# Kernel tuning notes

Measured on AMD Instinct MI355X. Metric: run time of the kernel, lower is better.

The kernel has to match this reference:

```python
import jax, jax.numpy as jnp
import numpy as np

N_EMBD = 1024
NUM_HEADS = 16
HEAD_SIZE = 64


def setup_inputs() -> dict:
    key = jax.random.key(0)
    ks = jax.random.split(key, 6)
    B, T, C, hs = 2, 2048, N_EMBD, HEAD_SIZE
    s = 0.02
    return {
        "x": jax.random.normal(ks[0], (B, T, C), dtype=jnp.float32),
        "Wk": jax.random.normal(ks[1], (hs, C), dtype=jnp.float32) * s,  # torch Linear weight [out,in]
        "Wv": jax.random.normal(ks[2], (hs, C), dtype=jnp.float32) * s,
        "Wq": jax.random.normal(ks[3], (C, C), dtype=jnp.float32) * s,
        "Wp": jax.random.normal(ks[4], (C, C), dtype=jnp.float32) * s,
        "bp": jax.random.normal(ks[5], (C,), dtype=jnp.float32) * s,
    }


def reference(x, Wk, Wv, Wq, Wp, bp):
    B, T, C = x.shape
    H, hs = NUM_HEADS, HEAD_SIZE
    k = x @ Wk.T                      # [B,T,hs]
    v = x @ Wv.T                      # [B,T,hs]
    q = x @ Wq.T                      # [B,T,C]
    # Faithful to torch: raw view of [B,T,C] -> [B,H,T,hs] (row-major reshape, not transpose)
    q = q.reshape(B, H, T, hs)
    k = k.reshape(B, 1, T, hs)
    v = v.reshape(B, 1, T, hs)
    att = jnp.einsum("bhqd,bhkd->bhqk", q, jnp.broadcast_to(k, (B, 1, T, hs))) * (hs ** -0.5)
    mask = jnp.tril(jnp.ones((T, T), dtype=bool))[None, None]  # [1,1,T,T]
    att = jnp.where(mask, att, -jnp.inf)
    att = jax.nn.softmax(att, axis=-1)
    y = jnp.einsum("bhqk,bhkd->bhqd", att, jnp.broadcast_to(v, (B, 1, T, hs)))  # [B,H,T,hs]
    y = jnp.transpose(y, (0, 2, 1, 3)).reshape(B, T, C)
    return y @ Wp.T + bp
```

## Files before the change

### kernel.cpp

```cpp
#include <hip/hip_runtime.h>
#include <cstddef>
#include <cstdint>

#define B_N 2
#define T_N 2048
#define C_N 1024
#define H_N 16
#define HS_N 64
#define M_N (B_N * T_N)

typedef __attribute__((ext_vector_type(8))) short bf16x8;
typedef __attribute__((ext_vector_type(4))) float f32x4;

#define QSCALE 0.18033688011112042f

__device__ __forceinline__ ushort f2bf(float f) {
    union { float f; uint32_t u; } v; v.f = f;
    uint32_t r = v.u + 0x7fffu + ((v.u >> 16) & 1u);
    return (ushort)(r >> 16);
}

#define GLL16(g, l)                                                         \
    __builtin_amdgcn_global_load_lds(                                       \
        (const __attribute__((address_space(1))) unsigned int*)(g),         \
        (__attribute__((address_space(3))) unsigned int*)(l), 16, 0, 0)

__global__ void cvt_all_kernel(const float* __restrict__ x,
                               const float* __restrict__ Wq,
                               const float* __restrict__ Wp,
                               const float* __restrict__ Wk,
                               const float* __restrict__ Wv,
                               ushort* __restrict__ xb,
                               ushort* __restrict__ Wqb,
                               ushort* __restrict__ Wpb,
                               ushort* __restrict__ Wkvb) {
    const int S0 = M_N * C_N / 4;
    const int S1 = S0 + C_N * C_N / 4;
    const int S2 = S1 + C_N * C_N / 4;
    const int S3 = S2 + HS_N * C_N / 4;
    const int S4 = S3 + HS_N * C_N / 4;
    const int stride = gridDim.x * blockDim.x;
    for (int i = blockIdx.x * blockDim.x + threadIdx.x; i < S4; i += stride) {
        const float* src; ushort* dst; int j; float sc = 1.f;
        if (i < S0)      { src = x;  dst = xb;   j = i; }
        else if (i < S1) { src = Wq; dst = Wqb;  j = i - S0; sc = QSCALE; }
        else if (i < S2) { src = Wp; dst = Wpb;  j = i - S1; }
        else if (i < S3) { src = Wk; dst = Wkvb; j = i - S2; }
        else             { src = Wv; dst = Wkvb + HS_N * C_N; j = i - S3; }
        const float4 f = ((const float4*)src)[j];
        ushort4 o;
        o.x = f2bf(f.x * sc); o.y = f2bf(f.y * sc);
        o.z = f2bf(f.z * sc); o.w = f2bf(f.w * sc);
        ((ushort4*)dst)[j] = o;
    }
}

template <bool BF16_OUT>
__global__ __launch_bounds__(256) void gemm_bf16_mfma(
    const ushort* __restrict__ A,
    const ushort* __restrict__ W,
    const float* __restrict__ bias,
    void* __restrict__ Cout,
    ushort* __restrict__ Cout2,
    int Nsplit, int N2, int K)
{
    __shared__ ushort As[128 * 64];
    __shared__ ushort Bs[64 * 64];
    const int m0 = blockIdx.x * 128;
    const int n0 = blockIdx.y * 64;
    const int tid = threadIdx.x;
    const int wid = tid >> 6;
    const int lane = tid & 63;
    const int ln = lane & 15;
    const int quad = lane >> 4;
    const int wm = wid >> 1, wn = wid & 1;

    f32x4 acc[4][2];
    #pragma unroll
    for (int i = 0; i < 4; ++i)
        #pragma unroll
        for (int j = 0; j < 2; ++j)
            acc[i][j] = (f32x4){0.f, 0.f, 0.f, 0.f};

    const int srow = lane >> 3;
    const int schk = (lane & 7) ^ srow;

    for (int k0 = 0; k0 < K; k0 += 64) {
        __syncthreads();
        #pragma unroll
        for (int t = 0; t < 4; ++t) {
            const int seg = wid * 4 + t;
            const int row = seg * 8 + srow;
            GLL16(A + (size_t)(m0 + row) * K + k0 + schk * 8, As + seg * 512);
        }
        #pragma unroll
        for (int t = 0; t < 2; ++t) {
            const int seg = wid * 2 + t;
            const int row = seg * 8 + srow;
            GLL16(W + (size_t)(n0 + row) * K + k0 + schk * 8, Bs + seg * 512);
        }
        __syncthreads();

        #pragma unroll
        for (int hh = 0; hh < 2; ++hh) {
            bf16x8 af[4], bf[2];
            const int sw = ln & 7;
            #pragma unroll
            for (int i = 0; i < 4; ++i) {
                const int row = wm * 64 + i * 16 + ln;
                af[i] = *(const bf16x8*)&As[row * 64 + (((hh * 4 + quad) ^ sw) * 8)];
            }
            #pragma unroll
            for (int j = 0; j < 2; ++j) {
                const int row = wn * 32 + j * 16 + ln;
                bf[j] = *(const bf16x8*)&Bs[row * 64 + (((hh * 4 + quad) ^ sw) * 8)];
            }
            #pragma unroll
            for (int i = 0; i < 4; ++i)
                #pragma unroll
                for (int j = 0; j < 2; ++j)
                    acc[i][j] = __builtin_amdgcn_mfma_f32_16x16x32_bf16(
                        af[i], bf[j], acc[i][j], 0, 0, 0);
        }
    }

    const bool side2 = (n0 >= Nsplit);
    #pragma unroll
    for (int i = 0; i < 4; ++i) {
        #pragma unroll
        for (int j = 0; j < 2; ++j) {
            const int col = n0 + wn * 32 + j * 16 + ln;
            const float bv = (!side2 && bias) ? bias[col] : 0.f;
            #pragma unroll
            for (int reg = 0; reg < 4; ++reg) {
                const int row = m0 + wm * 64 + i * 16 + quad * 4 + reg;
                const float v = acc[i][j][reg] + bv;
                if (side2)
                    Cout2[(size_t)row * N2 + (col - Nsplit)] = f2bf(v);
                else if (BF16_OUT)
                    ((ushort*)Cout)[(size_t)row * Nsplit + col] = f2bf(v);
                else
                    ((float*)Cout)[(size_t)row * Nsplit + col] = v;
            }
        }
    }
}

__global__ __launch_bounds__(256, 1) void attn_mfma_kernel(
    const ushort* __restrict__ qb,
    const ushort* __restrict__ kvb,
    ushort* __restrict__ yb)
{
    __shared__ ushort Ks[64][72];
    __shared__ ushort Vt[64][72];
    __shared__ ushort Ps[8][16][72];

    const int bh = blockIdx.x;
    const int b = bh >> 4, h = bh & 15;
    const int p = blockIdx.y;
    const int qB0 = (15 - p) * 128;
    const int qA0 = p * 128;
    const int tid = threadIdx.x;
    const int wid = tid >> 6;
    const int lane = tid & 63;
    const int ln = lane & 15;
    const int quad = lane >> 4;

    const ushort* qstrip = qb + (size_t)b * T_N * C_N + (size_t)h * T_N * HS_N;
    const int qbase[2] = {qB0, qA0};
    bf16x8 qf[2][2][2];
    #pragma unroll
    for (int t = 0; t < 2; ++t)
        #pragma unroll
        for (int s = 0; s < 2; ++s) {
            const size_t r = (size_t)(qbase[t] + wid * 32 + s * 16 + ln) * HS_N;
            qf[t][s][0] = *(const bf16x8*)(qstrip + r + quad * 8);
            qf[t][s][1] = *(const bf16x8*)(qstrip + r + 32 + quad * 8);
        }

    f32x4 o[2][2][4];
    float l_i[2][2] = {{0.f, 0.f}, {0.f, 0.f}};
    #pragma unroll
    for (int t = 0; t < 2; ++t)
        #pragma unroll
        for (int s = 0; s < 2; ++s)
            #pragma unroll
            for (int nt = 0; nt < 4; ++nt)
                o[t][s][nt] = (f32x4){0.f, 0.f, 0.f, 0.f};

    const ushort* kvbase = kvb + (size_t)b * T_N * 128;
    const int rs = tid >> 3;
    const int cs = tid & 7;

    int4 kc0, kc1, vc0, vc1;
    {
        const ushort* g0 = kvbase + (size_t)rs * 128 + cs * 8;
        kc0 = *(const int4*)g0;
        kc1 = *(const int4*)(g0 + 32 * 128);
        vc0 = *(const int4*)(g0 + 64);
        vc1 = *(const int4*)(g0 + 32 * 128 + 64);
    }

    bf16x8 kf[4][2], vf[4][2];

    auto tile_compute = [&](int t, int qt0, int k0) {
        #pragma unroll
        for (int s = 0; s < 2; ++s) {
            const int qg = qt0 + wid * 32 + s * 16 + ln;
            f32x4 sc[4];
            #pragma unroll
            for (int nt = 0; nt < 4; ++nt) {
                sc[nt] = (f32x4){0.f, 0.f, 0.f, 0.f};
                sc[nt] = __builtin_amdgcn_mfma_f32_16x16x32_bf16(
                    kf[nt][0], qf[t][s][0], sc[nt], 0, 0, 0);
                sc[nt] = __builtin_amdgcn_mfma_f32_16x16x32_bf16(
                    kf[nt][1], qf[t][s][1], sc[nt], 0, 0, 0);
            }
            const bool dg = (k0 + 63 > qt0 + wid * 32 + s * 16);
            const int plane = wid * 2 + s;
            #pragma unroll
            for (int nt = 0; nt < 4; ++nt) {
                ushort pk[4];
                #pragma unroll
                for (int reg = 0; reg < 4; ++reg) {
                    const int key = k0 + nt * 16 + quad * 4 + reg;
                    float sv = sc[nt][reg];
                    if (dg && key > qg) sv = -1e30f;
                    const float pe = __builtin_amdgcn_exp2f(sv);
                    l_i[t][s] += pe;
                    pk[reg] = f2bf(pe);
                }
                *(uint2*)&Ps[plane][ln][nt * 16 + quad * 4] = *(uint2*)pk;
            }
            #pragma unroll
            for (int ks2 = 0; ks2 < 2; ++ks2) {
                const bf16x8 pf =
                    *(const bf16x8*)&Ps[plane][ln][ks2 * 32 + quad * 8];
                #pragma unroll
                for (int nt = 0; nt < 4; ++nt)
                    o[t][s][nt] = __builtin_amdgcn_mfma_f32_16x16x32_bf16(
                        pf, vf[nt][ks2], o[t][s][nt], 0, 0, 0);
            }
        }
    };

    const int nkt = 2 * (16 - p);
    for (int kt = 0; kt < nkt; ++kt) {
        const int k0 = kt * 64;
        __syncthreads();
        *(int4*)&Ks[rs][cs * 8] = kc0;
        *(int4*)&Ks[rs + 32][cs * 8] = kc1;
        {
            const ushort* p0 = (const ushort*)&vc0;
            const ushort* p1 = (const ushort*)&vc1;
            const int pc0 = ((rs >> 3) ^ cs) * 8 + (rs & 7);
            const int pc1 = (((rs + 32) >> 3) ^ cs) * 8 + (rs & 7);
            #pragma unroll
            for (int i = 0; i < 8; ++i) {
                Vt[cs * 8 + i][pc0] = p0[i];
                Vt[cs * 8 + i][pc1] = p1[i];
            }
        }
        __syncthreads();
        if (kt + 1 < nkt) {
            const ushort* g0 = kvbase + (size_t)(k0 + 64 + rs) * 128 + cs * 8;
            kc0 = *(const int4*)g0;
            kc1 = *(const int4*)(g0 + 32 * 128);
            vc0 = *(const int4*)(g0 + 64);
            vc1 = *(const int4*)(g0 + 32 * 128 + 64);
        }
        #pragma unroll
        for (int nt = 0; nt < 4; ++nt) {
            kf[nt][0] = *(const bf16x8*)&Ks[nt * 16 + ln][quad * 8];
            kf[nt][1] = *(const bf16x8*)&Ks[nt * 16 + ln][32 + quad * 8];
            #pragma unroll
            for (int ks2 = 0; ks2 < 2; ++ks2) {
                const int vsw = (2 * nt + (ln >> 3)) & 7;
                vf[nt][ks2] =
                    *(const bf16x8*)&Vt[nt * 16 + ln][((quad + 4 * ks2) ^ vsw) * 8];
            }
        }
        tile_compute(0, qB0, k0);
        if (kt <= 2 * p + 1)
            tile_compute(1, qA0, k0);
    }

    #pragma unroll
    for (int t = 0; t < 2; ++t) {
        #pragma unroll
        for (int s = 0; s < 2; ++s) {
            float l = l_i[t][s];
            l += __shfl_xor(l, 16);
            l += __shfl_xor(l, 32);
            #pragma unroll
            for (int reg = 0; reg < 4; ++reg) {
                const float inv = 1.0f / __shfl(l, quad * 4 + reg);
                const int qg = qbase[t] + wid * 32 + s * 16 + quad * 4 + reg;
                ushort* yrow = yb + (size_t)b * T_N * C_N + (size_t)qg * C_N
                               + h * HS_N;
                #pragma unroll
                for (int nt = 0; nt < 4; ++nt)
                    yrow[nt * 16 + ln] = f2bf(o[t][s][nt][reg] * inv);
            }
        }
    }
}

extern "C" void kernel_launch(void* const* d_in, const int* in_sizes, int n_in,
                              void* d_out, int out_size, void* d_ws, size_t ws_size,
                              hipStream_t stream) {
    const float* x  = (const float*)d_in[0];
    const float* Wk = (const float*)d_in[1];
    const float* Wv = (const float*)d_in[2];
    const float* Wq = (const float*)d_in[3];
    const float* Wp = (const float*)d_in[4];
    const float* bp = (const float*)d_in[5];
    float* out = (float*)d_out;

    ushort* xb   = (ushort*)d_ws;
    ushort* qb   = xb   + (size_t)M_N * C_N;
    ushort* yb   = qb   + (size_t)M_N * C_N;
    ushort* kvb  = yb   + (size_t)M_N * C_N;
    ushort* Wqb  = kvb  + (size_t)M_N * 128;
    ushort* Wkvb = Wqb  + (size_t)C_N * C_N;
    ushort* Wpb  = Wkvb + (size_t)128 * C_N;

    cvt_all_kernel<<<1024, 256, 0, stream>>>(x, Wq, Wp, Wk, Wv,
                                             xb, Wqb, Wpb, Wkvb);

    gemm_bf16_mfma<true><<<dim3(M_N / 128, (C_N + 128) / 64), 256, 0, stream>>>(
        xb, Wqb, nullptr, qb, kvb, C_N, 128, C_N);

    attn_mfma_kernel<<<dim3(B_N * H_N, 8), 256, 0, stream>>>(qb, kvb, yb);

    gemm_bf16_mfma<false><<<dim3(M_N / 128, C_N / 64), 256, 0, stream>>>(
        yb, Wpb, bp, out, nullptr, C_N, 0, C_N);
}
```

Baseline: 169.2 us.

## Halve GEMM and attention tile sizes, emit pre-transposed V from projection GEMM

Both GEMMs shrink from 128x64 to 64x64 tiles, doubling the grid. The attention kernel moves from 256 to 512 blocks, each handling a balanced pair of 64-row query tiles, with two blocks per CU allowed. The QKV GEMM now writes K row-major and V already transposed ([b][d][t]), so attention loads V with plain vector stores instead of a scalar transpose into LDS. The intent is better CU occupancy and load balance on a small problem and less LDS transpose work, at the cost of less data reuse per tile and more global traffic for the GEMMs.

After: 154.3 us. -8.8%, faster.

```diff
diff --git a/kernel.cpp b/kernel.cpp
--- a/kernel.cpp
+++ b/kernel.cpp
@@ -55,18 +55,19 @@
     }
 }
 
-template <bool BF16_OUT>
-__global__ __launch_bounds__(256) void gemm_bf16_mfma(
+template <int MODE>
+__global__ __launch_bounds__(256) void gemm64(
     const ushort* __restrict__ A,
     const ushort* __restrict__ W,
     const float* __restrict__ bias,
     void* __restrict__ Cout,
-    ushort* __restrict__ Cout2,
-    int Nsplit, int N2, int K)
+    ushort* __restrict__ kb,
+    ushort* __restrict__ vbt,
+    int K)
 {
-    __shared__ ushort As[128 * 64];
+    __shared__ ushort As[64 * 64];
     __shared__ ushort Bs[64 * 64];
-    const int m0 = blockIdx.x * 128;
+    const int m0 = blockIdx.x * 64;
     const int n0 = blockIdx.y * 64;
     const int tid = threadIdx.x;
     const int wid = tid >> 6;
@@ -75,9 +76,9 @@
     const int quad = lane >> 4;
     const int wm = wid >> 1, wn = wid & 1;
 
-    f32x4 acc[4][2];
+    f32x4 acc[2][2];
     #pragma unroll
-    for (int i = 0; i < 4; ++i)
+    for (int i = 0; i < 2; ++i)
         #pragma unroll
         for (int j = 0; j < 2; ++j)
             acc[i][j] = (f32x4){0.f, 0.f, 0.f, 0.f};
@@ -88,26 +89,26 @@
     for (int k0 = 0; k0 < K; k0 += 64) {
         __syncthreads();
         #pragma unroll
-        for (int t = 0; t < 4; ++t) {
-            const int seg = wid * 4 + t;
-            const int row = seg * 8 + srow;
-            GLL16(A + (size_t)(m0 + row) * K + k0 + schk * 8, As + seg * 512);
-        }
-        #pragma unroll
         for (int t = 0; t < 2; ++t) {
             const int seg = wid * 2 + t;
-            const int row = seg * 8 + srow;
-            GLL16(W + (size_t)(n0 + row) * K + k0 + schk * 8, Bs + seg * 512);
+            GLL16(A + (size_t)(m0 + seg * 8 + srow) * K + k0 + schk * 8,
+                  As + seg * 512);
+        }
+        #pragma unroll
+        for (int t = 0; t < 2; ++t) {
+            const int seg = wid * 2 + t;
+            GLL16(W + (size_t)(n0 + seg * 8 + srow) * K + k0 + schk * 8,
+                  Bs + seg * 512);
         }
         __syncthreads();
 
         #pragma unroll
         for (int hh = 0; hh < 2; ++hh) {
-            bf16x8 af[4], bf[2];
+            bf16x8 af[2], bf[2];
             const int sw = ln & 7;
             #pragma unroll
-            for (int i = 0; i < 4; ++i) {
-                const int row = wm * 64 + i * 16 + ln;
+            for (int i = 0; i < 2; ++i) {
+                const int row = wm * 32 + i * 16 + ln;
                 af[i] = *(const bf16x8*)&As[row * 64 + (((hh * 4 + quad) ^ sw) * 8)];
             }
             #pragma unroll
@@ -116,7 +117,7 @@
                 bf[j] = *(const bf16x8*)&Bs[row * 64 + (((hh * 4 + quad) ^ sw) * 8)];
             }
             #pragma unroll
-            for (int i = 0; i < 4; ++i)
+            for (int i = 0; i < 2; ++i)
                 #pragma unroll
                 for (int j = 0; j < 2; ++j)
                     acc[i][j] = __builtin_amdgcn_mfma_f32_16x16x32_bf16(
@@ -124,42 +125,67 @@
         }
     }
 
-    const bool side2 = (n0 >= Nsplit);
+    if (MODE == 1 && n0 >= C_N) {
+        const int c2base = n0 - C_N;
+        const bool isV = (c2base >= 64);
+        #pragma unroll
+        for (int i = 0; i < 2; ++i) {
+            const int row0 = m0 + wm * 32 + i * 16 + quad * 4;
+            #pragma unroll
+            for (int j = 0; j < 2; ++j) {
+                const int c2 = c2base + wn * 32 + j * 16 + ln;
+                if (isV) {
+                    const int d = c2 - 64;
+                    const int b = row0 >> 11;
+                    const int t0 = row0 & 2047;
+                    ushort4 pk;
+                    pk.x = f2bf(acc[i][j][0]); pk.y = f2bf(acc[i][j][1]);
+                    pk.z = f2bf(acc[i][j][2]); pk.w = f2bf(acc[i][j][3]);
+                    *(ushort4*)&vbt[((size_t)b * 64 + d) * T_N + t0] = pk;
+                } else {
+                    #pragma unroll
+                    for (int reg = 0; reg < 4; ++reg)
+                        kb[(size_t)(row0 + reg) * 64 + c2] = f2bf(acc[i][j][reg]);
+                }
+            }
+        }
+        return;
+    }
+
     #pragma unroll
-    for (int i = 0; i < 4; ++i) {
+    for (int i = 0; i < 2; ++i) {
         #pragma unroll
         for (int j = 0; j < 2; ++j) {
             const int col = n0 + wn * 32 + j * 16 + ln;
-            const float bv = (!side2 && bias) ? bias[col] : 0.f;
+            const float bv = (MODE == 0) ? bias[col] : 0.f;
             #pragma unroll
             for (int reg = 0; reg < 4; ++reg) {
-                const int row = m0 + wm * 64 + i * 16 + quad * 4 + reg;
+                const int row = m0 + wm * 32 + i * 16 + quad * 4 + reg;
                 const float v = acc[i][j][reg] + bv;
-                if (side2)
-                    Cout2[(size_t)row * N2 + (col - Nsplit)] = f2bf(v);
-                else if (BF16_OUT)
-                    ((ushort*)Cout)[(size_t)row * Nsplit + col] = f2bf(v);
+                if (MODE == 0)
+                    ((float*)Cout)[(size_t)row * C_N + col] = v;
                 else
-                    ((float*)Cout)[(size_t)row * Nsplit + col] = v;
-            }
-        }
-    }
-}
-
-__global__ __launch_bounds__(256, 1) void attn_mfma_kernel(
+                    ((ushort*)Cout)[(size_t)row * C_N + col] = f2bf(v);
+            }
+        }
+    }
+}
+
+__global__ __launch_bounds__(256, 2) void attn_mfma_kernel(
     const ushort* __restrict__ qb,
-    const ushort* __restrict__ kvb,
+    const ushort* __restrict__ kb,
+    const ushort* __restrict__ vbt,
     ushort* __restrict__ yb)
 {
     __shared__ ushort Ks[64][72];
     __shared__ ushort Vt[64][72];
-    __shared__ ushort Ps[8][16][72];
+    __shared__ ushort Ps[4][16][72];
 
     const int bh = blockIdx.x;
     const int b = bh >> 4, h = bh & 15;
     const int p = blockIdx.y;
-    const int qB0 = (15 - p) * 128;
-    const int qA0 = p * 128;
+    const int qA0 = p * 64;
+    const int qB0 = (31 - p) * 64;
     const int tid = threadIdx.x;
     const int wid = tid >> 6;
     const int lane = tid & 63;
@@ -167,141 +193,119 @@
     const int quad = lane >> 4;
 
     const ushort* qstrip = qb + (size_t)b * T_N * C_N + (size_t)h * T_N * HS_N;
-    const int qbase[2] = {qB0, qA0};
-    bf16x8 qf[2][2][2];
+    const size_t rB = (size_t)(qB0 + wid * 16 + ln) * HS_N;
+    const size_t rA = (size_t)(qA0 + wid * 16 + ln) * HS_N;
+    bf16x8 qfB[2], qfA[2];
+    qfB[0] = *(const bf16x8*)(qstrip + rB + quad * 8);
+    qfB[1] = *(const bf16x8*)(qstrip + rB + 32 + quad * 8);
+    qfA[0] = *(const bf16x8*)(qstrip + rA + quad * 8);
+    qfA[1] = *(const bf16x8*)(qstrip + rA + 32 + quad * 8);
+
+    f32x4 oB[4], oA[4];
+    float lB = 0.f, lA = 0.f;
     #pragma unroll
-    for (int t = 0; t < 2; ++t)
-        #pragma unroll
-        for (int s = 0; s < 2; ++s) {
-            const size_t r = (size_t)(qbase[t] + wid * 32 + s * 16 + ln) * HS_N;
-            qf[t][s][0] = *(const bf16x8*)(qstrip + r + quad * 8);
-            qf[t][s][1] = *(const bf16x8*)(qstrip + r + 32 + quad * 8);
-        }
-
-    f32x4 o[2][2][4];
-    float l_i[2][2] = {{0.f, 0.f}, {0.f, 0.f}};
-    #pragma unroll
-    for (int t = 0; t < 2; ++t)
-        #pragma unroll
-        for (int s = 0; s < 2; ++s)
-            #pragma unroll
-            for (int nt = 0; nt < 4; ++nt)
-                o[t][s][nt] = (f32x4){0.f, 0.f, 0.f, 0.f};
-
-    const ushort* kvbase = kvb + (size_t)b * T_N * 128;
+    for (int nt = 0; nt < 4; ++nt) {
+        oB[nt] = (f32x4){0.f, 0.f, 0.f, 0.f};
+        oA[nt] = (f32x4){0.f, 0.f, 0.f, 0.f};
+    }
+
+    const ushort* kbase = kb + (size_t)b * T_N * HS_N;
+    const ushort* vtbase = vbt + (size_t)b * HS_N * T_N;
     const int rs = tid >> 3;
     const int cs = tid & 7;
 
     int4 kc0, kc1, vc0, vc1;
     {
-        const ushort* g0 = kvbase + (size_t)rs * 128 + cs * 8;
-        kc0 = *(const int4*)g0;
-        kc1 = *(const int4*)(g0 + 32 * 128);
-        vc0 = *(const int4*)(g0 + 64);
-        vc1 = *(const int4*)(g0 + 32 * 128 + 64);
+        kc0 = *(const int4*)(kbase + (size_t)rs * HS_N + cs * 8);
+        kc1 = *(const int4*)(kbase + (size_t)(rs + 32) * HS_N + cs * 8);
+        vc0 = *(const int4*)(vtbase + (size_t)rs * T_N + cs * 8);
+        vc1 = *(const int4*)(vtbase + (size_t)(rs + 32) * T_N + cs * 8);
     }
 
     bf16x8 kf[4][2], vf[4][2];
 
-    auto tile_compute = [&](int t, int qt0, int k0) {
-        #pragma unroll
-        for (int s = 0; s < 2; ++s) {
-            const int qg = qt0 + wid * 32 + s * 16 + ln;
-            f32x4 sc[4];
-            #pragma unroll
-            for (int nt = 0; nt < 4; ++nt) {
-                sc[nt] = (f32x4){0.f, 0.f, 0.f, 0.f};
-                sc[nt] = __builtin_amdgcn_mfma_f32_16x16x32_bf16(
-                    kf[nt][0], qf[t][s][0], sc[nt], 0, 0, 0);
-                sc[nt] = __builtin_amdgcn_mfma_f32_16x16x32_bf16(
-                    kf[nt][1], qf[t][s][1], sc[nt], 0, 0, 0);
-            }
-            const bool dg = (k0 + 63 > qt0 + wid * 32 + s * 16);
-            const int plane = wid * 2 + s;
-            #pragma unroll
-            for (int nt = 0; nt < 4; ++nt) {
-                ushort pk[4];
-                #pragma unroll
-                for (int reg = 0; reg < 4; ++reg) {
-                    const int key = k0 + nt * 16 + quad * 4 + reg;
-                    float sv = sc[nt][reg];
-                    if (dg && key > qg) sv = -1e30f;
-                    const float pe = __builtin_amdgcn_exp2f(sv);
-                    l_i[t][s] += pe;
-                    pk[reg] = f2bf(pe);
-                }
-                *(uint2*)&Ps[plane][ln][nt * 16 + quad * 4] = *(uint2*)pk;
-            }
-            #pragma unroll
-            for (int ks2 = 0; ks2 < 2; ++ks2) {
-                const bf16x8 pf =
-                    *(const bf16x8*)&Ps[plane][ln][ks2 * 32 + quad * 8];
-                #pragma unroll
-                for (int nt = 0; nt < 4; ++nt)
-                    o[t][s][nt] = __builtin_amdgcn_mfma_f32_16x16x32_bf16(
-                        pf, vf[nt][ks2], o[t][s][nt], 0, 0, 0);
-            }
+    auto tile_compute = [&](const bf16x8* qf, f32x4* o, float& l,
+                            int qt0, int k0) {
+        const int qs0 = qt0 + wid * 16;
+        const int qg = qs0 + ln;
+        f32x4 sc[4];
+        #pragma unroll
+        for (int nt = 0; nt < 4; ++nt) {
+            sc[nt] = (f32x4){0.f, 0.f, 0.f, 0.f};
+            sc[nt] = __builtin_amdgcn_mfma_f32_16x16x32_bf16(
+                kf[nt][0], qf[0], sc[nt], 0, 0, 0);
+            sc[nt] = __builtin_amdgcn_mfma_f32_16x16x32_bf16(
+                kf[nt][1], qf[1], sc[nt], 0, 0, 0);
+        }
+        const bool dg = (k0 + 63 > qs0);
+        #pragma unroll
+        for (int nt = 0; nt < 4; ++nt) {
+            ushort pk[4];
+            #pragma unroll
+            for (int reg = 0; reg < 4; ++reg) {
+                const int key = k0 + nt * 16 + quad * 4 + reg;
+                float sv = sc[nt][reg];
+                if (dg && key > qg) sv = -1e30f;
+                const float pe = __builtin_amdgcn_exp2f(sv);
+                l += pe;
+                pk[reg] = f2bf(pe);
+            }
+            *(uint2*)&Ps[wid][ln][nt * 16 + quad * 4] = *(const uint2*)pk;
+        }
+        #pragma unroll
+        for (int ks2 = 0; ks2 < 2; ++ks2) {
+            const bf16x8 pf = *(const bf16x8*)&Ps[wid][ln][ks2 * 32 + quad * 8];
+            #pragma unroll
+            for (int nt = 0; nt < 4; ++nt)
+                o[nt] = __builtin_amdgcn_mfma_f32_16x16x32_bf16(
+                    pf, vf[nt][ks2], o[nt], 0, 0, 0);
         }
     };
 
-    const int nkt = 2 * (16 - p);
+    const int nkt = 32 - p;
     for (int kt = 0; kt < nkt; ++kt) {
         const int k0 = kt * 64;
         __syncthreads();
         *(int4*)&Ks[rs][cs * 8] = kc0;
         *(int4*)&Ks[rs + 32][cs * 8] = kc1;
-        {
-            const ushort* p0 = (const ushort*)&vc0;
-            const ushort* p1 = (const ushort*)&vc1;
-            const int pc0 = ((rs >> 3) ^ cs) * 8 + (rs & 7);
-            const int pc1 = (((rs + 32) >> 3) ^ cs) * 8 + (rs & 7);
-            #pragma unroll
-            for (int i = 0; i < 8; ++i) {
-                Vt[cs * 8 + i][pc0] = p0[i];
-                Vt[cs * 8 + i][pc1] = p1[i];
-            }
-        }
+        *(int4*)&Vt[rs][cs * 8] = vc0;
+        *(int4*)&Vt[rs + 32][cs * 8] = vc1;
         __syncthreads();
         if (kt + 1 < nkt) {
-            const ushort* g0 = kvbase + (size_t)(k0 + 64 + rs) * 128 + cs * 8;
-            kc0 = *(const int4*)g0;
-            kc1 = *(const int4*)(g0 + 32 * 128);
-            vc0 = *(const int4*)(g0 + 64);
-            vc1 = *(const int4*)(g0 + 32 * 128 + 64);
+            const int kn = k0 + 64;
+            kc0 = *(const int4*)(kbase + (size_t)(kn + rs) * HS_N + cs * 8);
+            kc1 = *(const int4*)(kbase + (size_t)(kn + rs + 32) * HS_N + cs * 8);
+            vc0 = *(const int4*)(vtbase + (size_t)rs * T_N + kn + cs * 8);
+            vc1 = *(const int4*)(vtbase + (size_t)(rs + 32) * T_N + kn + cs * 8);
         }
         #pragma unroll
         for (int nt = 0; nt < 4; ++nt) {
             kf[nt][0] = *(const bf16x8*)&Ks[nt * 16 + ln][quad * 8];
             kf[nt][1] = *(const bf16x8*)&Ks[nt * 16 + ln][32 + quad * 8];
-            #pragma unroll
-            for (int ks2 = 0; ks2 < 2; ++ks2) {
-                const int vsw = (2 * nt + (ln >> 3)) & 7;
-                vf[nt][ks2] =
-                    *(const bf16x8*)&Vt[nt * 16 + ln][((quad + 4 * ks2) ^ vsw) * 8];
-            }
-        }
-        tile_compute(0, qB0, k0);
-        if (kt <= 2 * p + 1)
-            tile_compute(1, qA0, k0);
+            vf[nt][0] = *(const bf16x8*)&Vt[nt * 16 + ln][quad * 8];
+            vf[nt][1] = *(const bf16x8*)&Vt[nt * 16 + ln][32 + quad * 8];
+        }
+        tile_compute(qfB, oB, lB, qB0, k0);
+        if (kt <= p)
+            tile_compute(qfA, oA, lA, qA0, k0);
     }
 
     #pragma unroll
     for (int t = 0; t < 2; ++t) {
-        #pragma unroll
-        for (int s = 0; s < 2; ++s) {
-            float l = l_i[t][s];
-            l += __shfl_xor(l, 16);
-            l += __shfl_xor(l, 32);
-            #pragma unroll
-            for (int reg = 0; reg < 4; ++reg) {
-                const float inv = 1.0f / __shfl(l, quad * 4 + reg);
-                const int qg = qbase[t] + wid * 32 + s * 16 + quad * 4 + reg;
-                ushort* yrow = yb + (size_t)b * T_N * C_N + (size_t)qg * C_N
-                               + h * HS_N;
-                #pragma unroll
-                for (int nt = 0; nt < 4; ++nt)
-                    yrow[nt * 16 + ln] = f2bf(o[t][s][nt][reg] * inv);
-            }
+        float l = t ? lA : lB;
+        const f32x4* o = t ? oA : oB;
+        const int qt0 = t ? qA0 : qB0;
+        l += __shfl_xor(l, 16);
+        l += __shfl_xor(l, 32);
+        #pragma unroll
+        for (int reg = 0; reg < 4; ++reg) {
+            const float inv = 1.0f / __shfl(l, quad * 4 + reg);
+            const int qg = qt0 + wid * 16 + quad * 4 + reg;
+            ushort* yrow = yb + (size_t)b * T_N * C_N + (size_t)qg * C_N
+                           + h * HS_N;
+            #pragma unroll
+            for (int nt = 0; nt < 4; ++nt)
+                yrow[nt * 16 + ln] = f2bf(o[nt][reg] * inv);
         }
     }
 }
@@ -320,19 +324,20 @@
     ushort* xb   = (ushort*)d_ws;
     ushort* qb   = xb   + (size_t)M_N * C_N;
     ushort* yb   = qb   + (size_t)M_N * C_N;
-    ushort* kvb  = yb   + (size_t)M_N * C_N;
-    ushort* Wqb  = kvb  + (size_t)M_N * 128;
+    ushort* kbw  = yb   + (size_t)M_N * C_N;
+    ushort* vbt  = kbw  + (size_t)M_N * HS_N;
+    ushort* Wqb  = vbt  + (size_t)B_N * HS_N * T_N;
     ushort* Wkvb = Wqb  + (size_t)C_N * C_N;
     ushort* Wpb  = Wkvb + (size_t)128 * C_N;
 
     cvt_all_kernel<<<1024, 256, 0, stream>>>(x, Wq, Wp, Wk, Wv,
                                              xb, Wqb, Wpb, Wkvb);
 
-    gemm_bf16_mfma<true><<<dim3(M_N / 128, (C_N + 128) / 64), 256, 0, stream>>>(
-        xb, Wqb, nullptr, qb, kvb, C_N, 128, C_N);
-
-    attn_mfma_kernel<<<dim3(B_N * H_N, 8), 256, 0, stream>>>(qb, kvb, yb);
-
-    gemm_bf16_mfma<false><<<dim3(M_N / 128, C_N / 64), 256, 0, stream>>>(
-        yb, Wpb, bp, out, nullptr, C_N, 0, C_N);
-}
+    gemm64<1><<<dim3(M_N / 64, (C_N + 128) / 64), 256, 0, stream>>>(
+        xb, Wqb, nullptr, qb, kbw, vbt, C_N);
+
+    attn_mfma_kernel<<<dim3(B_N * H_N, 16), 256, 0, stream>>>(qb, kbw, vbt, yb);
+
+    gemm64<0><<<dim3(M_N / 64, C_N / 64), 256, 0, stream>>>(
+        yb, Wpb, bp, out, nullptr, nullptr, C_N);
+}
```
